# Kernel tuning notes

Measured on AMD Instinct MI355X. Metric: run time of the kernel, lower is better.

The kernel has to match this reference:

```python
import jax, jax.numpy as jnp
import numpy as np

HID = 64


def setup_inputs() -> dict:
    key = jax.random.key(0)
    k = jax.random.split(key, 7)
    B, T = 4096, 8192
    x = jax.random.normal(k[0], (B, T, 1), dtype=jnp.float32)
    # Kaiming-uniform-ish init scale; exact values irrelevant for correctness baseline
    W_in = jax.random.normal(k[1], (1, HID), dtype=jnp.float32) * 0.5
    b_in = jax.random.normal(k[2], (HID,), dtype=jnp.float32) * 0.1
    W_s = jax.random.normal(k[3], (HID, HID), dtype=jnp.float32) * (1.0 / np.sqrt(HID))
    b_s = jax.random.normal(k[4], (HID,), dtype=jnp.float32) * 0.1
    W_out = jax.random.normal(k[5], (HID, 1), dtype=jnp.float32) * (1.0 / np.sqrt(HID))
    b_out = jax.random.normal(k[6], (1,), dtype=jnp.float32) * 0.1
    return {"x": x, "W_in": W_in, "b_in": b_in, "W_s": W_s, "b_s": b_s,
            "W_out": W_out, "b_out": b_out}


def reference(x, W_in, b_in, W_s, b_s, W_out, b_out):
    B, T, _ = x.shape
    xt = jnp.swapaxes(x, 0, 1)  # [T, B, 1] -> scan over time

    def step(h, x_t):
        # input_proj on [B,1] -> [B,HID]; tiny GEMM per step (the recurrence is sequential)
        inp = x_t @ W_in + b_in
        h = jax.nn.gelu(h @ W_s + b_s + inp, approximate=False)  # torch GELU = exact erf
        return h, None

    h0 = jnp.zeros((B, HID), dtype=x.dtype)
    h_final, _ = jax.lax.scan(step, h0, xt)
    return h_final @ W_out + b_out  # [B, 1]
```

## Files before the change

kernel.cpp:

```cpp
#include <hip/hip_runtime.h>
#include <cstdint>
#include <cstddef>

#define HID 64
#define RPG 16
#define HSTR 72
#define XSTR 68

typedef short bf16x8 __attribute__((ext_vector_type(8)));
typedef float f32x4 __attribute__((ext_vector_type(4)));

__device__ __forceinline__ float fast_gelu(float z) {
    float u = z * 0.70710678118654752f;
    float a = __builtin_fabsf(u);
    float t = __builtin_amdgcn_rcpf(__builtin_fmaf(0.3275911f, a, 1.0f));
    float s = u * 1.20112240878645f;
    float e = __builtin_amdgcn_exp2f(-(s * s));
    float p =                   1.061405429f;
    p = __builtin_fmaf(p, t, -1.453152027f);
    p = __builtin_fmaf(p, t,  1.421413741f);
    p = __builtin_fmaf(p, t, -0.284496736f);
    p = __builtin_fmaf(p, t,  0.254829592f);
    p = p * t;
    float er = __builtin_fmaf(-p, e, 1.0f);
    er = __builtin_copysignf(er, u);
    float zh = 0.5f * z;
    return __builtin_fmaf(zh, er, zh);
}

__device__ __forceinline__ ushort bf16_hi(float f) {
    return (ushort)(__float_as_uint(f) >> 16);
}
__device__ __forceinline__ float bf16_f(ushort u) {
    return __uint_as_float(((unsigned)u) << 16);
}

#define PKHI(b_, a_) __builtin_amdgcn_perm((b_), (a_), 0x07060302u)

#define STEP(RHI, RLO, WHI, WLO, XB) { \
    const bf16x8 Hhi0 = *reinterpret_cast<const bf16x8*>(RHI); \
    const bf16x8 Hhi1 = *reinterpret_cast<const bf16x8*>((RHI) + 32); \
    const bf16x8 Hlo0 = *reinterpret_cast<const bf16x8*>(RLO); \
    const bf16x8 Hlo1 = *reinterpret_cast<const bf16x8*>((RLO) + 32); \
    const f32x4 zz = {0.f, 0.f, 0.f, 0.f}; \
    f32x4 ahh = __builtin_amdgcn_mfma_f32_16x16x32_bf16(Whi0, Hhi0, zz, 0, 0, 0); \
    f32x4 ac1 = __builtin_amdgcn_mfma_f32_16x16x32_bf16(Whi0, Hlo0, zz, 0, 0, 0); \
    f32x4 ac2 = __builtin_amdgcn_mfma_f32_16x16x32_bf16(Wlo0, Hhi0, zz, 0, 0, 0); \
    ahh = __builtin_amdgcn_mfma_f32_16x16x32_bf16(Whi1, Hhi1, ahh, 0, 0, 0); \
    ac1 = __builtin_amdgcn_mfma_f32_16x16x32_bf16(Whi1, Hlo1, ac1, 0, 0, 0); \
    ac2 = __builtin_amdgcn_mfma_f32_16x16x32_bf16(Wlo1, Hhi1, ac2, 0, 0, 0); \
    const float z0 = (ahh[0] + ac1[0]) + (ac2[0] + __builtin_fmaf((XB), win0, cb0)); \
    const float z1 = (ahh[1] + ac1[1]) + (ac2[1] + __builtin_fmaf((XB), win1, cb1)); \
    const float z2 = (ahh[2] + ac1[2]) + (ac2[2] + __builtin_fmaf((XB), win2, cb2)); \
    const float z3 = (ahh[3] + ac1[3]) + (ac2[3] + __builtin_fmaf((XB), win3, cb3)); \
    const float h0 = fast_gelu(z0); \
    const float h1 = fast_gelu(z1); \
    const float h2 = fast_gelu(z2); \
    const float h3 = fast_gelu(z3); \
    const unsigned hb0 = __float_as_uint(h0), hb1 = __float_as_uint(h1); \
    const unsigned hb2 = __float_as_uint(h2), hb3 = __float_as_uint(h3); \
    uint2 hpk; hpk.x = PKHI(hb1, hb0); hpk.y = PKHI(hb3, hb2); \
    *(WHI) = hpk; \
    const unsigned lb0 = __float_as_uint(h0 - __uint_as_float(hb0 & 0xffff0000u)); \
    const unsigned lb1 = __float_as_uint(h1 - __uint_as_float(hb1 & 0xffff0000u)); \
    const unsigned lb2 = __float_as_uint(h2 - __uint_as_float(hb2 & 0xffff0000u)); \
    const unsigned lb3 = __float_as_uint(h3 - __uint_as_float(hb3 & 0xffff0000u)); \
    uint2 lpk; lpk.x = PKHI(lb1, lb0); lpk.y = PKHI(lb3, lb2); \
    *(WLO) = lpk; \
    __syncthreads(); }

__global__ __launch_bounds__(256, 1)
void ssm_kernel(const float* __restrict__ x,
                const float* __restrict__ W_in,
                const float* __restrict__ b_in,
                const float* __restrict__ W_s,
                const float* __restrict__ b_s,
                const float* __restrict__ W_out,
                const float* __restrict__ b_out,
                float* __restrict__ out,
                int B, int T) {
    __shared__ ushort hlds[2][2][RPG * HSTR];
    __shared__ float  xlds[RPG][XSTR];

    const int tid  = threadIdx.x;
    const int g    = tid >> 6;
    const int lane = tid & 63;
    const int q    = lane >> 4;
    const int rr   = lane & 15;
    const int bA   = blockIdx.x * RPG;
    const int cq   = 16 * g + 4 * q;

    if (bA >= B) return;

    bf16x8 Whi0, Whi1, Wlo0, Wlo1;
    const int wcol = 16 * g + rr;
#pragma unroll
    for (int e = 0; e < 8; ++e) {
        {   const float wf = W_s[(8 * q + e) * HID + wcol];
            const ushort hi = bf16_hi(wf);
            Whi0[e] = (short)hi;
            Wlo0[e] = (short)bf16_hi(wf - bf16_f(hi)); }
        {   const float wf = W_s[(32 + 8 * q + e) * HID + wcol];
            const ushort hi = bf16_hi(wf);
            Whi1[e] = (short)hi;
            Wlo1[e] = (short)bf16_hi(wf - bf16_f(hi)); }
    }
    asm volatile("" : "+v"(Whi0), "+v"(Whi1), "+v"(Wlo0), "+v"(Wlo1));

    const float win0 = W_in[cq + 0], win1 = W_in[cq + 1];
    const float win2 = W_in[cq + 2], win3 = W_in[cq + 3];
    const float cb0 = b_in[cq + 0] + b_s[cq + 0];
    const float cb1 = b_in[cq + 1] + b_s[cq + 1];
    const float cb2 = b_in[cq + 2] + b_s[cq + 2];
    const float cb3 = b_in[cq + 3] + b_s[cq + 3];

    {
        ushort* p = &hlds[0][0][0];
        for (int i = tid; i < 2 * RPG * HSTR; i += 256) p[i] = 0;
    }

    const ushort* const rhiA = &hlds[0][0][rr * HSTR + 8 * q];
    const ushort* const rloA = &hlds[0][1][rr * HSTR + 8 * q];
    const ushort* const rhiB = &hlds[1][0][rr * HSTR + 8 * q];
    const ushort* const rloB = &hlds[1][1][rr * HSTR + 8 * q];
    uint2* const whiA = reinterpret_cast<uint2*>(&hlds[0][0][rr * HSTR + cq]);
    uint2* const wloA = reinterpret_cast<uint2*>(&hlds[0][1][rr * HSTR + cq]);
    uint2* const whiB = reinterpret_cast<uint2*>(&hlds[1][0][rr * HSTR + cq]);
    uint2* const wloB = reinterpret_cast<uint2*>(&hlds[1][1][rr * HSTR + cq]);

    const int nch = T >> 6;

    for (int tc = 0; tc < nch; ++tc) {
        {
            const int row = tid >> 4;
            const int ch  = tid & 15;
            const float4 xg = *reinterpret_cast<const float4*>(
                &x[(size_t)(bA + row) * (size_t)T + (size_t)(tc * 64 + ch * 4)]);
            *reinterpret_cast<float4*>(&xlds[row][ch * 4]) = xg;
        }
        __syncthreads();

#pragma unroll 1
        for (int t4 = 0; t4 < 16; ++t4) {
            const f32x4 xq = *reinterpret_cast<const f32x4*>(&xlds[rr][t4 * 4]);
            STEP(rhiA, rloA, whiB, wloB, xq[0])
            STEP(rhiB, rloB, whiA, wloA, xq[1])
            STEP(rhiA, rloA, whiB, wloB, xq[2])
            STEP(rhiB, rloB, whiA, wloA, xq[3])
        }
    }

    if (g == 0) {
        const int r  = lane >> 2;
        const int p4 = lane & 3;
        const ushort* hp = &hlds[0][0][r * HSTR + p4 * 16];
        const ushort* lp = &hlds[0][1][r * HSTR + p4 * 16];
        float s = 0.f;
#pragma unroll
        for (int j = 0; j < 16; ++j)
            s = __builtin_fmaf(bf16_f(hp[j]) + bf16_f(lp[j]), W_out[p4 * 16 + j], s);
        s += __shfl_xor(s, 1, 64);
        s += __shfl_xor(s, 2, 64);
        if (p4 == 0) out[bA + r] = s + b_out[0];
    }
}

extern "C" void kernel_launch(void* const* d_in, const int* in_sizes, int n_in,
                              void* d_out, int out_size, void* d_ws, size_t ws_size,
                              hipStream_t stream) {
    const float* x     = (const float*)d_in[0];
    const float* W_in  = (const float*)d_in[1];
    const float* b_in  = (const float*)d_in[2];
    const float* W_s   = (const float*)d_in[3];
    const float* b_s   = (const float*)d_in[4];
    const float* W_out = (const float*)d_in[5];
    const float* b_out = (const float*)d_in[6];
    float* out = (float*)d_out;

    const int B = out_size;
    const int T = in_sizes[0] / B;

    const int blocks = B / RPG;
    ssm_kernel<<<blocks, 256, 0, stream>>>(
        x, W_in, b_in, W_s, b_s, W_out, b_out, out, B, T);
}
```

Before: 2.896 ms.

## Pack two independent row groups per 512-thread block and fold bias into MFMA

Each block now runs two independent 16-row recurrences, one per set of 4 wavefronts, with separate LDS state buffers but a shared block-wide barrier. The input projection plus bias is passed as the initial accumulator of one MFMA chain instead of being added after the MFMAs. The intent is to let one group's MFMA and GELU latency hide behind the other's. The cost is that the grid is halved to 128 blocks, so fewer CUs may be used on this part, and both groups now wait on each other's barriers.

Result: slower. 3.891 ms (+34.4%).

```diff
diff --git a/kernel.cpp b/kernel.cpp
--- a/kernel.cpp
+++ b/kernel.cpp
@@ -4,6 +4,7 @@
 
 #define HID 64
 #define RPG 16
+#define NGRP 2
 #define HSTR 72
 #define XSTR 68
 
@@ -42,17 +43,21 @@
     const bf16x8 Hhi1 = *reinterpret_cast<const bf16x8*>((RHI) + 32); \
     const bf16x8 Hlo0 = *reinterpret_cast<const bf16x8*>(RLO); \
     const bf16x8 Hlo1 = *reinterpret_cast<const bf16x8*>((RLO) + 32); \
+    const f32x4 bi = { __builtin_fmaf((XB), win0, cb0), \
+                       __builtin_fmaf((XB), win1, cb1), \
+                       __builtin_fmaf((XB), win2, cb2), \
+                       __builtin_fmaf((XB), win3, cb3) }; \
     const f32x4 zz = {0.f, 0.f, 0.f, 0.f}; \
     f32x4 ahh = __builtin_amdgcn_mfma_f32_16x16x32_bf16(Whi0, Hhi0, zz, 0, 0, 0); \
-    f32x4 ac1 = __builtin_amdgcn_mfma_f32_16x16x32_bf16(Whi0, Hlo0, zz, 0, 0, 0); \
+    f32x4 ac1 = __builtin_amdgcn_mfma_f32_16x16x32_bf16(Whi0, Hlo0, bi, 0, 0, 0); \
     f32x4 ac2 = __builtin_amdgcn_mfma_f32_16x16x32_bf16(Wlo0, Hhi0, zz, 0, 0, 0); \
     ahh = __builtin_amdgcn_mfma_f32_16x16x32_bf16(Whi1, Hhi1, ahh, 0, 0, 0); \
     ac1 = __builtin_amdgcn_mfma_f32_16x16x32_bf16(Whi1, Hlo1, ac1, 0, 0, 0); \
     ac2 = __builtin_amdgcn_mfma_f32_16x16x32_bf16(Wlo1, Hhi1, ac2, 0, 0, 0); \
-    const float z0 = (ahh[0] + ac1[0]) + (ac2[0] + __builtin_fmaf((XB), win0, cb0)); \
-    const float z1 = (ahh[1] + ac1[1]) + (ac2[1] + __builtin_fmaf((XB), win1, cb1)); \
-    const float z2 = (ahh[2] + ac1[2]) + (ac2[2] + __builtin_fmaf((XB), win2, cb2)); \
-    const float z3 = (ahh[3] + ac1[3]) + (ac2[3] + __builtin_fmaf((XB), win3, cb3)); \
+    const float z0 = (ahh[0] + ac1[0]) + ac2[0]; \
+    const float z1 = (ahh[1] + ac1[1]) + ac2[1]; \
+    const float z2 = (ahh[2] + ac1[2]) + ac2[2]; \
+    const float z3 = (ahh[3] + ac1[3]) + ac2[3]; \
     const float h0 = fast_gelu(z0); \
     const float h1 = fast_gelu(z1); \
     const float h2 = fast_gelu(z2); \
@@ -69,7 +74,7 @@
     *(WLO) = lpk; \
     __syncthreads(); }
 
-__global__ __launch_bounds__(256, 1)
+__global__ __launch_bounds__(512, 2)
 void ssm_kernel(const float* __restrict__ x,
                 const float* __restrict__ W_in,
                 const float* __restrict__ b_in,
@@ -79,15 +84,17 @@
                 const float* __restrict__ b_out,
                 float* __restrict__ out,
                 int B, int T) {
-    __shared__ ushort hlds[2][2][RPG * HSTR];
-    __shared__ float  xlds[RPG][XSTR];
+    __shared__ ushort hlds[NGRP][2][2][RPG * HSTR];
+    __shared__ float  xlds[NGRP * RPG][XSTR];
 
     const int tid  = threadIdx.x;
-    const int g    = tid >> 6;
+    const int ww   = tid >> 6;
+    const int grp  = ww >> 2;
+    const int g    = ww & 3;
     const int lane = tid & 63;
     const int q    = lane >> 4;
     const int rr   = lane & 15;
-    const int bA   = blockIdx.x * RPG;
+    const int bA   = blockIdx.x * (NGRP * RPG);
     const int cq   = 16 * g + 4 * q;
 
     if (bA >= B) return;
@@ -115,18 +122,19 @@
     const float cb3 = b_in[cq + 3] + b_s[cq + 3];
 
     {
-        ushort* p = &hlds[0][0][0];
-        for (int i = tid; i < 2 * RPG * HSTR; i += 256) p[i] = 0;
+        ushort* p = &hlds[0][0][0][0];
+        for (int i = tid; i < NGRP * 2 * 2 * RPG * HSTR; i += 512) p[i] = 0;
     }
 
-    const ushort* const rhiA = &hlds[0][0][rr * HSTR + 8 * q];
-    const ushort* const rloA = &hlds[0][1][rr * HSTR + 8 * q];
-    const ushort* const rhiB = &hlds[1][0][rr * HSTR + 8 * q];
-    const ushort* const rloB = &hlds[1][1][rr * HSTR + 8 * q];
-    uint2* const whiA = reinterpret_cast<uint2*>(&hlds[0][0][rr * HSTR + cq]);
-    uint2* const wloA = reinterpret_cast<uint2*>(&hlds[0][1][rr * HSTR + cq]);
-    uint2* const whiB = reinterpret_cast<uint2*>(&hlds[1][0][rr * HSTR + cq]);
-    uint2* const wloB = reinterpret_cast<uint2*>(&hlds[1][1][rr * HSTR + cq]);
+    const ushort* const rhiA = &hlds[grp][0][0][rr * HSTR + 8 * q];
+    const ushort* const rloA = &hlds[grp][0][1][rr * HSTR + 8 * q];
+    const ushort* const rhiB = &hlds[grp][1][0][rr * HSTR + 8 * q];
+    const ushort* const rloB = &hlds[grp][1][1][rr * HSTR + 8 * q];
+    uint2* const whiA = reinterpret_cast<uint2*>(&hlds[grp][0][0][rr * HSTR + cq]);
+    uint2* const wloA = reinterpret_cast<uint2*>(&hlds[grp][0][1][rr * HSTR + cq]);
+    uint2* const whiB = reinterpret_cast<uint2*>(&hlds[grp][1][0][rr * HSTR + cq]);
+    uint2* const wloB = reinterpret_cast<uint2*>(&hlds[grp][1][1][rr * HSTR + cq]);
+    const float* const xrow = &xlds[RPG * grp + rr][0];
 
     const int nch = T >> 6;
 
@@ -142,7 +150,7 @@
 
 #pragma unroll 1
         for (int t4 = 0; t4 < 16; ++t4) {
-            const f32x4 xq = *reinterpret_cast<const f32x4*>(&xlds[rr][t4 * 4]);
+            const f32x4 xq = *reinterpret_cast<const f32x4*>(xrow + t4 * 4);
             STEP(rhiA, rloA, whiB, wloB, xq[0])
             STEP(rhiB, rloB, whiA, wloA, xq[1])
             STEP(rhiA, rloA, whiB, wloB, xq[2])
@@ -150,18 +158,18 @@
         }
     }
 
-    if (g == 0) {
+    if ((ww & 3) == 0) {
         const int r  = lane >> 2;
         const int p4 = lane & 3;
-        const ushort* hp = &hlds[0][0][r * HSTR + p4 * 16];
-        const ushort* lp = &hlds[0][1][r * HSTR + p4 * 16];
+        const ushort* hp = &hlds[grp][0][0][r * HSTR + p4 * 16];
+        const ushort* lp = &hlds[grp][0][1][r * HSTR + p4 * 16];
         float s = 0.f;
 #pragma unroll
         for (int j = 0; j < 16; ++j)
             s = __builtin_fmaf(bf16_f(hp[j]) + bf16_f(lp[j]), W_out[p4 * 16 + j], s);
         s += __shfl_xor(s, 1, 64);
         s += __shfl_xor(s, 2, 64);
-        if (p4 == 0) out[bA + r] = s + b_out[0];
+        if (p4 == 0) out[bA + RPG * grp + r] = s + b_out[0];
     }
 }
 
@@ -180,7 +188,8 @@
     const int B = out_size;
     const int T = in_sizes[0] / B;
 
-    const int blocks = B / RPG;
-    ssm_kernel<<<blocks, 256, 0, stream>>>(
+    const int rows_per_block = NGRP * RPG;
+    const int blocks = (B + rows_per_block - 1) / rows_per_block;
+    ssm_kernel<<<blocks, 512, 0, stream>>>(
         x, W_in, b_in, W_s, b_s, W_out, b_out, out, B, T);
 }
```
